# Kernel optimization log

Measured on AMD Instinct MI355X. Metric: run time of the kernel, lower is better.

## Reference

```python
import jax, jax.numpy as jnp
import numpy as np

VOCAB = 128000
D = 256
N_BUBBLES = 256
N_EQ_STEPS = 5
SEQ_LEN = 512
ETA = 0.1      # relaxation rate toward input
KAPPA = 0.05   # mean-field coupling between bubbles


def setup_inputs() -> dict:
    key = jax.random.key(0)
    k1, k2, k3 = jax.random.split(key, 3)
    embed = jax.random.normal(k1, (VOCAB, D), dtype=jnp.float32)
    bubbles = jax.random.normal(k2, (N_BUBBLES, D), dtype=jnp.float32)
    memory_decay_base = jnp.asarray(0.8, dtype=jnp.float32)
    novelty_sensitivity = jnp.asarray(1.0, dtype=jnp.float32)
    tokens = jax.random.randint(k3, (SEQ_LEN,), 0, VOCAB, dtype=jnp.int64)
    return {"embed": embed, "bubbles": bubbles,
            "memory_decay_base": memory_decay_base,
            "novelty_sensitivity": novelty_sensitivity,
            "tokens": tokens}


def _foam_forward(x, bubbles):
    """x: [d]. Equilibrate bubble states, build density matrix, eigen-spectrum."""
    s = bubbles  # [n_bubbles, d]
    for _ in range(N_EQ_STEPS):  # fixed small hyperparam loop
        s = s + ETA * (x[None, :] - s) + KAPPA * (s.mean(axis=0, keepdims=True) - s)
        s = s / (jnp.linalg.norm(s, axis=-1, keepdims=True) + 1e-10)
    rho = (s.T @ s) / s.shape[0]  # [d, d] PSD, trace ~ 1
    w = jnp.linalg.eigvalsh(rho)  # ascending eigenvalues [d]
    w = jnp.clip(w, 0.0)
    output_dist = w / (w.sum() + 1e-10)
    return s, output_dist


def reference(embed, bubbles, memory_decay_base, novelty_sensitivity, tokens):
    sens = jnp.abs(novelty_sensitivity)

    def step(memory, tok):
        x = embed[tok]                      # [d]
        mem_mean = memory.mean(axis=0)      # [d]
        mem_norm = jnp.linalg.norm(mem_mean) + 1e-10
        x_norm = jnp.linalg.norm(x) + 1e-10
        novelty = jnp.where(mem_norm > 1e-8,
                            1.0 - jnp.dot(x, mem_mean) / (x_norm * mem_norm),
                            1.0)
        decay = jax.nn.sigmoid(memory_decay_base - sens * novelty)
        x_with_memory = x + decay * mem_mean
        eq, output_dist = _foam_forward(x_with_memory, bubbles)
        memory = decay * memory + (1.0 - decay) * eq
        return memory, output_dist

    memory0 = jnp.zeros_like(bubbles)  # [n_bubbles, d]
    _, dists = jax.lax.scan(step, memory0, tokens)
    return dists  # [seq_len, d] per-step eigenvalue distributions of rho
```

## Files before the change

kernel.cpp:

```cpp
#include <hip/hip_runtime.h>
#include <hip/hip_fp16.h>
#include <math.h>

#define SEQ 512
#define ETA 0.1f
#define KAPPA 0.05f
#define AA 0.85f

typedef _Float16 f16x8 __attribute__((ext_vector_type(8)));
typedef float f32x4 __attribute__((ext_vector_type(4)));

#define WS_G    ((size_t)0)
#define WS_GD   ((size_t)65536)
#define WS_M0   ((size_t)65792)
#define WS_BX   ((size_t)66048)
#define WS_X2   ((size_t)197120)
#define WS_ZS   ((size_t)197632)
#define WS_YS   ((size_t)328704)
#define WS_GS   ((size_t)459776)
#define WS_HS   ((size_t)984064)
#define WS_ALS  ((size_t)986112)
#define WS_BETS ((size_t)1117184)
#define WS_CT   ((size_t)1772544)

__device__ __forceinline__ float wred_sum(float v) {
#pragma unroll
  for (int m = 1; m < 64; m <<= 1) v += __shfl_xor(v, m, 64);
  return v;
}
__device__ __forceinline__ float wred_min(float v) {
#pragma unroll
  for (int m = 1; m < 64; m <<= 1) v = fminf(v, __shfl_xor(v, m, 64));
  return v;
}
__device__ __forceinline__ float wred_max(float v) {
#pragma unroll
  for (int m = 1; m < 64; m <<= 1) v = fmaxf(v, __shfl_xor(v, m, 64));
  return v;
}
__device__ __forceinline__ float psum32(float v) {
  v += __shfl_xor(v, 2, 64);
  v += __shfl_xor(v, 4, 64);
  v += __shfl_xor(v, 8, 64);
  v += __shfl_xor(v, 16, 64);
  v += __shfl_xor(v, 32, 64);
  return v;
}
__device__ __forceinline__ float rfl(float x) {
  return __builtin_bit_cast(float, __builtin_amdgcn_readfirstlane(__builtin_bit_cast(int, x)));
}

#define G_LIST(X) X(0) X(1) X(2) X(3) X(4) X(5) X(6) X(7) \
                  X(8) X(9) X(10) X(11) X(12) X(13) X(14) X(15) \
                  X(16) X(17) X(18) X(19) X(20) X(21) X(22) X(23) \
                  X(24) X(25) X(26) X(27) X(28) X(29) X(30) X(31)

__global__ void k0_gram(const float* __restrict__ B, float* __restrict__ ws) {
  float* G = ws + WS_G;
  float* Gd = ws + WS_GD;
  __shared__ float bi[256];
  const int i = blockIdx.x, j = threadIdx.x;
  bi[j] = B[(size_t)i * 256 + j];
  __syncthreads();
  float a0 = 0.f, a1 = 0.f, a2 = 0.f, a3 = 0.f;
#pragma unroll
  for (int c = 0; c < 256; c += 4) {
    float4 b4 = *(const float4*)&B[(size_t)j * 256 + c];
    a0 = fmaf(bi[c + 0], b4.x, a0);
    a1 = fmaf(bi[c + 1], b4.y, a1);
    a2 = fmaf(bi[c + 2], b4.z, a2);
    a3 = fmaf(bi[c + 3], b4.w, a3);
  }
  float acc = (a0 + a1) + (a2 + a3);
  G[(size_t)i * 256 + j] = acc;
  if (i == j) Gd[i] = acc;
}

__global__ void k0_m0(const float* __restrict__ B, float* __restrict__ ws) {
  float* M0 = ws + WS_M0;
  const int d = threadIdx.x;
  float acc = 0.f;
  for (int i = 0; i < 256; ++i) acc += B[(size_t)i * 256 + d];
  M0[d] = acc * (1.0f / 256.0f);
}

__global__ void k0_bx(const float* __restrict__ B, const float* __restrict__ embed,
                      const int* __restrict__ toks, float* __restrict__ ws) {
  float* BX = ws + WS_BX;
  float* X2 = ws + WS_X2;
  __shared__ float xs[256];
  __shared__ float red[4];
  const int t = blockIdx.x, i = threadIdx.x;
  const int lane = i & 63, wid = i >> 6;
  const int tok = toks[t];
  float xv = embed[(size_t)tok * 256 + i];
  xs[i] = xv;
  float p = wred_sum(xv * xv);
  if (lane == 0) red[wid] = p;
  __syncthreads();
  if (i == 0) X2[t] = red[0] + red[1] + red[2] + red[3];
  float a0 = 0.f, a1 = 0.f, a2 = 0.f, a3 = 0.f;
#pragma unroll
  for (int c = 0; c < 256; c += 4) {
    float4 b4 = *(const float4*)&B[(size_t)i * 256 + c];
    a0 = fmaf(xs[c + 0], b4.x, a0);
    a1 = fmaf(xs[c + 1], b4.y, a1);
    a2 = fmaf(xs[c + 2], b4.z, a2);
    a3 = fmaf(xs[c + 3], b4.w, a3);
  }
  BX[(size_t)t * 256 + i] = (a0 + a1) + (a2 + a3);
}

__global__ __launch_bounds__(512)
__attribute__((amdgpu_waves_per_eu(2, 2)))
void k1_seq(
    const float* __restrict__ embed, const int* __restrict__ toks,
    const float* __restrict__ mdbp, const float* __restrict__ sensp,
    float* __restrict__ ws) {
  const int tid = threadIdx.x;
  const int lane = tid & 63;
  const int i = tid >> 1, h = tid & 1;
  const float* G = ws + WS_G;
  const float* Gd = ws + WS_GD;
  const float* BX = ws + WS_BX;
  const float* X2 = ws + WS_X2;
  float* ZS = ws + WS_ZS;
  float* YS = ws + WS_YS;
  float* GS = ws + WS_GS;
  float* HS = ws + WS_HS;
  float* ALS = ws + WS_ALS;
  float* BETS = ws + WS_BETS;

  __shared__ __align__(16) float gcur[256];
  __shared__ float dresb[2][8];
  __shared__ float bbarb[2][8];

  const float4* gp = (const float4*)(G + (size_t)i * 256 + (size_t)h * 128);
#define DECLG(J) float4 Gr##J = gp[J];
  G_LIST(DECLG)
#undef DECLG
  const float Gdi = Gd[i];
  const float mdb = rfl(mdbp[0]);
  const float sens = fabsf(rfl(sensp[0]));

  float q0i;
  {
    float s = 0.f;
#define SUMG(J) s += (Gr##J.x + Gr##J.y) + (Gr##J.z + Gr##J.w);
    G_LIST(SUMG)
#undef SUMG
    s += __shfl_xor(s, 1, 64);
    q0i = s * (1.0f / 256.0f);
  }

  float x_c = embed[(size_t)toks[0] * 256 + i];
  float bx_c = BX[i];
  float x2_c = rfl(X2[0]);

  if (tid < 16) dresb[tid >> 3][tid & 7] = 0.f;
  else if (tid < 32) bbarb[(tid - 16) >> 3][tid & 7] = 0.f;
  __syncthreads();
  {
    float v = h ? (bx_c * (1.0f / 256.0f)) : (q0i * (1.0f / 256.0f));
    v = psum32(v);
    if (lane == h) atomicAdd(&dresb[0][h], v);
  }
  __syncthreads();
  const float c00 = rfl(dresb[0][0]);
  float mbx = rfl(dresb[0][1]);

  float Zi = 0.f, yi = 0.f, wi = 0.f;
  float mm2 = 0.f, mw = 0.f, dotxm = 0.f;

  float dec = 1.0f / (1.0f + expf(-(mdb - sens)));
  float od = 1.0f - dec;
  float ri = bx_c;
  float XM2 = x2_c;
  float mean_r = mbx;
  if (h == 0) ZS[i] = 0.f;
  else YS[i] = x_c;

  float gh[6], Ggh[6], hhv[6], bmat[5], xmm[5], alpha;
  gh[0] = 1.0f / 256.0f; Ggh[0] = q0i; hhv[0] = 0.f;
  {
    const float xmm0 = mean_r;
    const float tki = ETA * ri + KAPPA * q0i;
    const float CC00 = (ETA * ETA) * XM2 + 2.f * (ETA * KAPPA) * xmm0 +
                       (KAPPA * KAPPA) * c00;
    const float n2 = fmaxf(AA * AA * Gdi + 2.f * AA * tki + CC00, 0.f);
    const float inv = 1.0f / (sqrtf(n2) + 1e-10f);
    bmat[0] = inv; alpha = AA * inv; xmm[0] = xmm0;
  }
  if (h == 0) gcur[i] = alpha;
  {
    float bv = h ? 0.f : bmat[0];
    bv = psum32(bv);
    if (lane == 0) atomicAdd(&bbarb[1][0], bv);
  }
  __syncthreads();
  int pq = 1;

#pragma unroll 1
  for (int t = 0; t < SEQ; ++t) {
    const int tn = (t + 1 < SEQ) ? (t + 1) : t;
    const int tokn = toks[tn];
    const float x_n = embed[(size_t)tokn * 256 + i];
    const float bx_n = BX[(size_t)tn * 256 + i];
    const float x2_n = rfl(X2[tn]);
    float q5sav = 0.f;

#pragma unroll
    for (int k = 1; k <= 5; ++k) {
      if (tid < 8) dresb[1 - pq][tid] = 0.f;
      else if (tid < 16) bbarb[1 - pq][tid - 8] = 0.f;
      float4 av = {0.f, 0.f, 0.f, 0.f};
      const float4* gc4 = (const float4*)&gcur[h * 128];
#define MVG(J) { const float4 g4 = gc4[J]; \
      av.x = fmaf(Gr##J.x, g4.x, av.x); av.y = fmaf(Gr##J.y, g4.y, av.y); \
      av.z = fmaf(Gr##J.z, g4.z, av.z); av.w = fmaf(Gr##J.w, g4.w, av.w); }
      G_LIST(MVG)
#undef MVG
      float M = (av.x + av.y) + (av.z + av.w);
      M += __shfl_xor(M, 1, 64);
      float hk = 0.f, gk = alpha * (1.0f / 256.0f), Ggk = M * (1.0f / 256.0f);
#pragma unroll
      for (int l = 0; l < 5; ++l)
        if (l < k) {
          const float bb = rfl(bbarb[pq][l]) * (1.0f / 256.0f);
          hk += bb * (ETA + KAPPA * hhv[l]);
          gk = fmaf(KAPPA * bb, gh[l], gk);
          Ggk = fmaf(KAPPA * bb, Ggh[l], Ggk);
        }
      const float qk = Ggk + hk * ri;
      gh[k] = gk; Ggh[k] = Ggk; hhv[k] = hk;
      if (k <= 4) {
        if (h == 1) GS[(size_t)(k - 1) * (SEQ * 256) + (size_t)t * 256 + i] = gk;
        if (tid == 0) HS[(size_t)(k - 1) * SEQ + t] = hk;
      }
      float vv[8];
      if (k < 5) {
#pragma unroll
        for (int l = 0; l < 8; ++l) {
          if (l <= k) vv[l] = gk * (Ggh[l] + hhv[l] * ri);
          else if (l == k + 1) vv[l] = ri * gk;
          else vv[l] = 0.f;
        }
      } else {
        q5sav = qk;
        vv[0] = gk * qk;
        vv[1] = ri * gk;
        vv[2] = wi * gk;
        vv[3] = qk * (1.0f / 256.0f);
        vv[4] = bx_n * Zi + x_n * yi;
        vv[5] = bx_n * gk;
        vv[6] = x_n * x_c;
        vv[7] = bx_n * (1.0f / 256.0f);
      }
      const int nv = (k < 5) ? (k + 2) : 8;
      const int ulim = (k < 5) ? (k + 2) : 4;
      float red4[4] = {0.f, 0.f, 0.f, 0.f};
#pragma unroll
      for (int u = 0; u < 4; ++u)
        if (u < ulim) red4[u] = psum32(h ? vv[4 + u] : vv[u]);
      if (lane == h) {
#pragma unroll
        for (int u = 0; u < 4; ++u) {
          const int sl = h * 4 + u;
          if (sl < nv) atomicAdd(&dresb[pq][sl], red4[u]);
        }
      }
      __syncthreads();

      if (k < 5) {
        float dres[7];
#pragma unroll
        for (int l = 0; l < 7; ++l)
          if (l <= k + 1) dres[l] = rfl(dresb[pq][l]);
        const float xmmk = dres[k + 1] + hk * XM2;
        const float tki = ETA * ri + KAPPA * qk;
        float sc = alpha * tki;
#pragma unroll
        for (int jj = 0; jj < 4; ++jj)
          if (jj < k) {
            const float MMjk = dres[jj] + hk * xmm[jj];
            const float CCjk = (ETA * ETA) * XM2 + (ETA * KAPPA) * (xmm[jj] + xmmk) +
                               (KAPPA * KAPPA) * MMjk;
            sc = fmaf(bmat[jj], CCjk, sc);
          }
        const float MMkk = dres[k] + hk * xmmk;
        const float CCkk = (ETA * ETA) * XM2 + 2.f * (ETA * KAPPA) * xmmk +
                           (KAPPA * KAPPA) * MMkk;
        const float n2 = fmaxf(AA * AA + 2.f * AA * sc + CCkk, 0.f);
        const float inv = 1.0f / (sqrtf(n2) + 1e-10f);
#pragma unroll
        for (int jj = 0; jj < 4; ++jj)
          if (jj < k) bmat[jj] *= AA * inv;
        bmat[k] = inv;
        alpha *= AA * inv;
        xmm[k] = xmmk;
        if (k == 4) {
          if (h == 1) {
            ALS[(size_t)t * 256 + i] = alpha;
            BETS[(size_t)1 * (SEQ * 256) + (size_t)t * 256 + i] = bmat[1];
            BETS[(size_t)3 * (SEQ * 256) + (size_t)t * 256 + i] = bmat[3];
          } else {
            BETS[(size_t)0 * (SEQ * 256) + (size_t)t * 256 + i] = bmat[0];
            BETS[(size_t)2 * (SEQ * 256) + (size_t)t * 256 + i] = bmat[2];
            BETS[(size_t)4 * (SEQ * 256) + (size_t)t * 256 + i] = bmat[4];
          }
        }
        if (h == 0) gcur[i] = alpha;
        float rb0 = h ? bmat[1] : bmat[0];
        float rb1 = h ? ((k >= 3) ? bmat[3] : 0.f) : ((k >= 2) ? bmat[2] : 0.f);
        float rb2 = h ? 0.f : ((k >= 4) ? bmat[4] : 0.f);
        rb0 = psum32(rb0);
        if (k >= 2) rb1 = psum32(rb1);
        if (k >= 4) rb2 = psum32(rb2);
        if (lane == h) {
          atomicAdd(&bbarb[1 - pq][h], rb0);
          if (2 + h <= k) atomicAdd(&bbarb[1 - pq][2 + h], rb1);
          if (4 + h <= k) atomicAdd(&bbarb[1 - pq][4 + h], rb2);
        }
        __syncthreads();
        pq ^= 1;
      } else {
        float dr[8];
#pragma unroll
        for (int l = 0; l < 8; ++l) dr[l] = rfl(dresb[pq][l]);
        const float h5 = hhv[5];
        const float g5 = gh[5];
        const float q5 = q5sav;
        const float xmm5 = dr[1] + h5 * XM2;
        const float m52 = dr[0] + h5 * xmm5;
        const float cmm5 = dr[2] + h5 * (dotxm + dec * mm2);
        const float lamc = dec * (1.0f + od * h5);
        Zi = lamc * Zi + od * g5;
        yi = lamc * yi + od * h5 * x_c;
        wi = dec * wi + od * q5;
        mm2 = fmaxf(dec * dec * mm2 + 2.f * dec * od * cmm5 + od * od * m52, 0.f);
        mw = dec * mw + od * dr[3];
        dotxm = lamc * dr[4] + od * (dr[5] + h5 * dr[6]);
        mbx = dr[7];
        x_c = x_n; bx_c = bx_n; x2_c = x2_n;
        const float memnorm = sqrtf(mm2) + 1e-10f;
        const float xnorm = sqrtf(x2_c) + 1e-10f;
        const float nov = (memnorm > 1e-8f) ? (1.0f - dotxm / (xnorm * memnorm)) : 1.0f;
        dec = 1.0f / (1.0f + expf(-(mdb - sens * nov)));
        od = 1.0f - dec;
        ri = bx_c + dec * wi;
        XM2 = x2_c + 2.f * dec * dotxm + dec * dec * mm2;
        mean_r = mbx + dec * mw;
        if (t + 1 < SEQ) {
          if (h == 0) ZS[(size_t)(t + 1) * 256 + i] = dec * Zi;
          else YS[(size_t)(t + 1) * 256 + i] = x_c + dec * yi;
        }
        const float xmm0 = mean_r;
        const float tki = ETA * ri + KAPPA * q0i;
        const float CC00 = (ETA * ETA) * XM2 + 2.f * (ETA * KAPPA) * xmm0 +
                           (KAPPA * KAPPA) * c00;
        const float n2 = fmaxf(AA * AA * Gdi + 2.f * AA * tki + CC00, 0.f);
        const float inv = 1.0f / (sqrtf(n2) + 1e-10f);
        bmat[0] = inv; alpha = AA * inv; xmm[0] = xmm0;
        if (h == 0) gcur[i] = alpha;
        float bv = h ? 0.f : bmat[0];
        bv = psum32(bv);
        if (lane == 0) atomicAdd(&bbarb[1 - pq][0], bv);
        __syncthreads();
        pq ^= 1;
      }
    }
  }
}

__global__ void k15_cvec(const float* __restrict__ B, float* __restrict__ ws) {
  const float* ZS = ws + WS_ZS;
  const float* YS = ws + WS_YS;
  const float* GS = ws + WS_GS;
  const float* HS = ws + WS_HS;
  const float* M0 = ws + WS_M0;
  float* CT = ws + WS_CT;
  const int t = blockIdx.x, d = threadIdx.x;
  __shared__ float zs[256], g1[256], g2[256], g3[256], g4[256];
  zs[d] = ZS[(size_t)t * 256 + d];
  g1[d] = GS[0 * (SEQ * 256) + (size_t)t * 256 + d];
  g2[d] = GS[1 * (SEQ * 256) + (size_t)t * 256 + d];
  g3[d] = GS[2 * (SEQ * 256) + (size_t)t * 256 + d];
  g4[d] = GS[3 * (SEQ * 256) + (size_t)t * 256 + d];
  __syncthreads();
  float xa = 0.f, b1 = 0.f, b2 = 0.f, b3 = 0.f, b4 = 0.f;
  for (int ii = 0; ii < 256; ++ii) {
    const float Bv = B[(size_t)ii * 256 + d];
    xa = fmaf(zs[ii], Bv, xa);
    b1 = fmaf(g1[ii], Bv, b1);
    b2 = fmaf(g2[ii], Bv, b2);
    b3 = fmaf(g3[ii], Bv, b3);
    b4 = fmaf(g4[ii], Bv, b4);
  }
  const float xm = YS[(size_t)t * 256 + d] + xa;
  float* ctt = CT + (size_t)t * 1280;
  ctt[0 * 256 + d] = ETA * xm + KAPPA * M0[d];
  const float h1 = HS[0 * SEQ + t], h2 = HS[1 * SEQ + t];
  const float h3 = HS[2 * SEQ + t], h4 = HS[3 * SEQ + t];
  ctt[1 * 256 + d] = (ETA + KAPPA * h1) * xm + KAPPA * b1;
  ctt[2 * 256 + d] = (ETA + KAPPA * h2) * xm + KAPPA * b2;
  ctt[3 * 256 + d] = (ETA + KAPPA * h3) * xm + KAPPA * b3;
  ctt[4 * 256 + d] = (ETA + KAPPA * h4) * xm + KAPPA * b4;
}

__global__ __launch_bounds__(1024, 4) void k2_eig(
    const float* __restrict__ B, const float* __restrict__ ws,
    float* __restrict__ out) {
  const int t = blockIdx.x;
  const int tid = threadIdx.x;
  const int lane = tid & 63, wid = tid >> 6;
  const float* CT = ws + WS_CT + (size_t)t * 1280;
  const float* ALS = ws + WS_ALS + (size_t)t * 256;
  const float* BETS = ws + WS_BETS;

  __shared__ __align__(16) unsigned char bigbuf[135168];
  _Float16* sT = (_Float16*)bigbuf;
  float* pk = (float*)bigbuf;
  __shared__ __align__(16) float ct[1280];
  __shared__ float vx[256], pv[256], qv[256];
  __shared__ float dd[256], ee[256], e2[256], lamv[256];
  __shared__ float red[16];

  for (int idx = tid; idx < 1280; idx += 1024) ct[idx] = CT[idx];
  __syncthreads();

  {
    const int r = tid >> 2, q = tid & 3;
    const float al = ALS[r];
    const float be0 = BETS[(size_t)0 * (SEQ * 256) + (size_t)t * 256 + r];
    const float be1 = BETS[(size_t)1 * (SEQ * 256) + (size_t)t * 256 + r];
    const float be2 = BETS[(size_t)2 * (SEQ * 256) + (size_t)t * 256 + r];
    const float be3 = BETS[(size_t)3 * (SEQ * 256) + (size_t)t * 256 + r];
    const float be4 = BETS[(size_t)4 * (SEQ * 256) + (size_t)t * 256 + r];
#pragma unroll
    for (int j4 = 0; j4 < 16; ++j4) {
      const int d0 = q * 64 + j4 * 4;
      const float4 Bv = *(const float4*)&B[(size_t)r * 256 + d0];
      const float4 c0 = *(const float4*)&ct[0 * 256 + d0];
      const float4 c1 = *(const float4*)&ct[1 * 256 + d0];
      const float4 c2 = *(const float4*)&ct[2 * 256 + d0];
      const float4 c3 = *(const float4*)&ct[3 * 256 + d0];
      const float4 c4 = *(const float4*)&ct[4 * 256 + d0];
      const float s0 = al * Bv.x + be0 * c0.x + be1 * c1.x + be2 * c2.x + be3 * c3.x + be4 * c4.x;
      const float s1 = al * Bv.y + be0 * c0.y + be1 * c1.y + be2 * c2.y + be3 * c3.y + be4 * c4.y;
      const float s2 = al * Bv.z + be0 * c0.z + be1 * c1.z + be2 * c2.z + be3 * c3.z + be4 * c4.z;
      const float s3 = al * Bv.w + be0 * c0.w + be1 * c1.w + be2 * c2.w + be3 * c3.w + be4 * c4.w;
      sT[(size_t)(d0 + 0) * 264 + r] = (_Float16)s0;
      sT[(size_t)(d0 + 1) * 264 + r] = (_Float16)s1;
      sT[(size_t)(d0 + 2) * 264 + r] = (_Float16)s2;
      sT[(size_t)(d0 + 3) * 264 + r] = (_Float16)s3;
    }
  }
  __syncthreads();

  f32x4 acc[4][4];
#pragma unroll
  for (int ti = 0; ti < 4; ++ti)
#pragma unroll
    for (int tj = 0; tj < 4; ++tj) {
      f32x4 z = {0.f, 0.f, 0.f, 0.f};
      acc[ti][tj] = z;
    }
  {
    const int Ib = (wid >> 2) * 4, Jb = (wid & 3) * 4;
    const int mr = lane & 15, kg = lane >> 4;
#pragma unroll 1
    for (int kb = 0; kb < 8; ++kb) {
      const int ko = kb * 32 + kg * 8;
      f16x8 aF[4], bF[4];
#pragma unroll
      for (int ti = 0; ti < 4; ++ti)
        aF[ti] = *(const f16x8*)&sT[(size_t)((Ib + ti) * 16 + mr) * 264 + ko];
#pragma unroll
      for (int tj = 0; tj < 4; ++tj)
        bF[tj] = *(const f16x8*)&sT[(size_t)((Jb + tj) * 16 + mr) * 264 + ko];
#pragma unroll
      for (int ti = 0; ti < 4; ++ti)
#pragma unroll
        for (int tj = 0; tj < 4; ++tj)
          acc[ti][tj] = __builtin_amdgcn_mfma_f32_16x16x32_f16(aF[ti], bF[tj], acc[ti][tj], 0, 0, 0);
    }
  }
  __syncthreads();
  {
    const int Ib = (wid >> 2) * 4, Jb = (wid & 3) * 4;
    const int cn = lane & 15, rg = lane >> 4;
#pragma unroll
    for (int ti = 0; ti < 4; ++ti)
#pragma unroll
      for (int tj = 0; tj < 4; ++tj) {
        const int C = (Jb + tj) * 16 + cn;
        const int Rb = (Ib + ti) * 16 + rg * 4;
#pragma unroll
        for (int rr = 0; rr < 4; ++rr) {
          const int R = Rb + rr;
          if (R >= C) pk[R * (R + 1) / 2 + C] = acc[ti][tj][rr] * (1.0f / 256.0f);
        }
      }
  }
  __syncthreads();

#pragma unroll 1
  for (int j = 0; j < 254; ++j) {
    const int m = 255 - j;
    const float x0 = pk[(j + 1) * (j + 2) / 2 + j];
    float ps = 0.f;
    if (tid < m) {
      const int gr = j + 1 + tid;
      const float xv_ = pk[gr * (gr + 1) / 2 + j];
      vx[tid] = xv_;
      ps = xv_ * xv_;
    }
    ps = wred_sum(ps);
    if (lane == 0) red[wid] = ps;
    __syncthreads();
    float sig2 = 0.f;
#pragma unroll
    for (int w = 0; w < 16; ++w) sig2 += red[w];
    const float sig = sqrtf(sig2);
    const float sg = (x0 >= 0.f) ? 1.f : -1.f;
    const bool live = (sig2 > 1e-26f);
    const float beta = live ? (1.0f / (sig * (sig + fabsf(x0)))) : 0.f;
    const float v0 = live ? (x0 + sg * sig) : 0.f;
    if (tid == 0) {
      dd[j] = pk[j * (j + 1) / 2 + j];
      ee[j] = live ? (-sg * sig) : x0;
      vx[0] = v0;
    }
    __syncthreads();
    {
      const int ri_ = tid >> 2, qd = tid & 3;
      float acc2 = 0.f;
      if (ri_ < m) {
        const int gr = j + 1 + ri_;
        const int c0 = (m * qd) >> 2, c1 = (m * (qd + 1)) >> 2;
        const int rowbase = gr * (gr + 1) / 2 + (j + 1);
        const int clend = min(c1, ri_ + 1);
        for (int c = c0; c < clend; ++c) acc2 = fmaf(pk[rowbase + c], vx[c], acc2);
        const int cu = max(c0, ri_ + 1);
        if (cu < c1) {
          int gc = j + 1 + cu;
          int ub = gc * (gc + 1) / 2 + gr;
          int stp = gc + 1;
          for (int c = cu; c < c1; ++c) { acc2 = fmaf(pk[ub], vx[c], acc2); ub += stp; ++stp; }
        }
      }
      acc2 += __shfl_xor(acc2, 1, 64);
      acc2 += __shfl_xor(acc2, 2, 64);
      float vpp = 0.f;
      if ((tid & 3) == 0 && (tid >> 2) < m) { pv[tid >> 2] = acc2; vpp = acc2 * vx[tid >> 2]; }
      vpp = wred_sum(vpp);
      if (lane == 0) red[wid] = vpp;
    }
    __syncthreads();
    float vtp = 0.f;
#pragma unroll
    for (int w = 0; w < 16; ++w) vtp += red[w];
    const float gamma = 0.5f * beta * beta * vtp;
    if (tid < m) qv[tid] = beta * pv[tid] - gamma * vx[tid];
    __syncthreads();
    {
      const int Q = tid >> 2, qd = tid & 3;
      const int i2 = m - 1 - Q;
      if (Q <= i2 && Q < m) {
        {
          const int gr = j + 1 + Q;
          const int rb = gr * (gr + 1) / 2 + (j + 1);
          const float vi = vx[Q], qi = qv[Q];
          const int cs = (qd * (Q + 1)) >> 2, ce = ((qd + 1) * (Q + 1)) >> 2;
          for (int c = cs; c < ce; ++c) pk[rb + c] -= vi * qv[c] + qi * vx[c];
        }
        if (i2 > Q) {
          const int gr = j + 1 + i2;
          const int rb = gr * (gr + 1) / 2 + (j + 1);
          const float vi = vx[i2], qi = qv[i2];
          const int cs = (qd * (i2 + 1)) >> 2, ce = ((qd + 1) * (i2 + 1)) >> 2;
          for (int c = cs; c < ce; ++c) pk[rb + c] -= vi * qv[c] + qi * vx[c];
        }
      }
    }
    __syncthreads();
  }
  if (tid == 0) {
    dd[254] = pk[254 * 255 / 2 + 254];
    dd[255] = pk[255 * 256 / 2 + 255];
    ee[254] = pk[255 * 256 / 2 + 254];
    ee[255] = 0.f;
  }
  __syncthreads();
  if (tid < 256) e2[tid] = ee[tid] * ee[tid];
  __syncthreads();
  float glo = 1e30f, ghi = -1e30f;
  if (tid < 256) {
    const float rad = fabsf(ee[tid]) + ((tid > 0) ? fabsf(ee[tid - 1]) : 0.f);
    glo = dd[tid] - rad;
    ghi = dd[tid] + rad;
  }
  {
    float v = wred_min(glo);
    if (lane == 0) red[wid] = v;
    __syncthreads();
    float lo0 = 1e30f;
#pragma unroll
    for (int w = 0; w < 16; ++w) lo0 = fminf(lo0, red[w]);
    __syncthreads();
    v = wred_max(ghi);
    if (lane == 0) red[wid] = v;
    __syncthreads();
    float hi0 = -1e30f;
#pragma unroll
    for (int w = 0; w < 16; ++w) hi0 = fmaxf(hi0, red[w]);
    lo0 -= 1e-3f + 1e-3f * fabsf(lo0);
    hi0 += 1e-3f + 1e-3f * fabsf(hi0);
    if (tid < 256) {
      float lo = lo0, hi = hi0;
      for (int it = 0; it < 21; ++it) {
        const float x = 0.5f * (lo + hi);
        int cnt = 0;
        float qq = dd[0] - x;
        cnt += (qq < 0.f);
        for (int ii = 1; ii < 256; ++ii) {
          float dn = qq;
          if (fabsf(dn) < 1e-25f) dn = (dn < 0.f) ? -1e-25f : 1e-25f;
          qq = (dd[ii] - x) - e2[ii - 1] * __builtin_amdgcn_rcpf(dn);
          cnt += (qq < 0.f);
        }
        if (cnt >= tid + 1) hi = x; else lo = x;
      }
      lamv[tid] = fmaxf(0.5f * (lo + hi), 0.f);
    }
  }
  __syncthreads();
  float sv = (tid < 256) ? lamv[tid] : 0.f;
  sv = wred_sum(sv);
  if (lane == 0) red[wid] = sv;
  __syncthreads();
  float S = 0.f;
#pragma unroll
  for (int w = 0; w < 16; ++w) S += red[w];
  if (tid < 256) out[(size_t)t * 256 + tid] = lamv[tid] / (S + 1e-10f);
}

extern "C" void kernel_launch(void* const* d_in, const int* in_sizes, int n_in,
                              void* d_out, int out_size, void* d_ws, size_t ws_size,
                              hipStream_t stream) {
  const float* embed = (const float*)d_in[0];
  const float* B = (const float*)d_in[1];
  const float* mdb = (const float*)d_in[2];
  const float* sens = (const float*)d_in[3];
  const int* toks = (const int*)d_in[4];
  float* out = (float*)d_out;
  float* ws = (float*)d_ws;

  k0_gram<<<dim3(256), dim3(256), 0, stream>>>(B, ws);
  k0_m0<<<dim3(1), dim3(256), 0, stream>>>(B, ws);
  k0_bx<<<dim3(SEQ), dim3(256), 0, stream>>>(B, embed, toks, ws);
  k1_seq<<<dim3(1), dim3(512), 0, stream>>>(embed, toks, mdb, sens, ws);
  k15_cvec<<<dim3(SEQ), dim3(256), 0, stream>>>(B, ws);
  k2_eig<<<dim3(SEQ), dim3(1024), 0, stream>>>(B, ws, out);
}
```

Baseline: 10.63 ms.

## Split sequential kernel's Gram matvec across four thread groups with deferred partial sums

The single-block sequential kernel grows from 512 to 1024 threads, and each row of the register-resident Gram matrix is split into four 64-column chunks instead of two halves. Partial matvec results go to a shared buffer and are combined only after the existing barrier. The per-step reduction algebra is reworked to use these partial sums, so the cross-lane shuffle on the critical path goes away. This halves register pressure per thread and shortens each matvec, but adds more wave reductions and atomics and doubles the waves taking part in every barrier.

```diff
diff --git a/kernel.cpp b/kernel.cpp
--- a/kernel.cpp
+++ b/kernel.cpp
@@ -38,22 +38,12 @@
   for (int m = 1; m < 64; m <<= 1) v = fmaxf(v, __shfl_xor(v, m, 64));
   return v;
 }
-__device__ __forceinline__ float psum32(float v) {
-  v += __shfl_xor(v, 2, 64);
-  v += __shfl_xor(v, 4, 64);
-  v += __shfl_xor(v, 8, 64);
-  v += __shfl_xor(v, 16, 64);
-  v += __shfl_xor(v, 32, 64);
-  return v;
-}
 __device__ __forceinline__ float rfl(float x) {
   return __builtin_bit_cast(float, __builtin_amdgcn_readfirstlane(__builtin_bit_cast(int, x)));
 }
 
 #define G_LIST(X) X(0) X(1) X(2) X(3) X(4) X(5) X(6) X(7) \
-                  X(8) X(9) X(10) X(11) X(12) X(13) X(14) X(15) \
-                  X(16) X(17) X(18) X(19) X(20) X(21) X(22) X(23) \
-                  X(24) X(25) X(26) X(27) X(28) X(29) X(30) X(31)
+                  X(8) X(9) X(10) X(11) X(12) X(13) X(14) X(15)
 
 __global__ void k0_gram(const float* __restrict__ B, float* __restrict__ ws) {
   float* G = ws + WS_G;
@@ -111,15 +101,15 @@
   BX[(size_t)t * 256 + i] = (a0 + a1) + (a2 + a3);
 }
 
-__global__ __launch_bounds__(512)
-__attribute__((amdgpu_waves_per_eu(2, 2)))
+__global__ __launch_bounds__(1024)
+__attribute__((amdgpu_waves_per_eu(4, 4)))
 void k1_seq(
     const float* __restrict__ embed, const int* __restrict__ toks,
     const float* __restrict__ mdbp, const float* __restrict__ sensp,
     float* __restrict__ ws) {
   const int tid = threadIdx.x;
   const int lane = tid & 63;
-  const int i = tid >> 1, h = tid & 1;
+  const int i = tid & 255, c = tid >> 8;
   const float* G = ws + WS_G;
   const float* Gd = ws + WS_GD;
   const float* BX = ws + WS_BX;
@@ -132,10 +122,11 @@
   float* BETS = ws + WS_BETS;
 
   __shared__ __align__(16) float gcur[256];
+  __shared__ float pbuf[4][264];
   __shared__ float dresb[2][8];
   __shared__ float bbarb[2][8];
 
-  const float4* gp = (const float4*)(G + (size_t)i * 256 + (size_t)h * 128);
+  const float4* gp = (const float4*)(G + (size_t)i * 256 + (size_t)c * 64);
 #define DECLG(J) float4 Gr##J = gp[J];
   G_LIST(DECLG)
 #undef DECLG
@@ -143,27 +134,33 @@
   const float mdb = rfl(mdbp[0]);
   const float sens = fabsf(rfl(sensp[0]));
 
-  float q0i;
+  float Gghp0;
   {
     float s = 0.f;
 #define SUMG(J) s += (Gr##J.x + Gr##J.y) + (Gr##J.z + Gr##J.w);
     G_LIST(SUMG)
 #undef SUMG
-    s += __shfl_xor(s, 1, 64);
-    q0i = s * (1.0f / 256.0f);
-  }
+    Gghp0 = s * (1.0f / 256.0f);
+  }
+  if (tid < 8) dresb[0][tid] = 0.f;
+  else if (tid < 16) dresb[1][tid - 8] = 0.f;
+  else if (tid < 24) bbarb[0][tid - 16] = 0.f;
+  else if (tid < 32) bbarb[1][tid - 24] = 0.f;
+  pbuf[c][i] = Gghp0;
+  __syncthreads();
+  const float q0i = pbuf[0][i] + pbuf[1][i] + pbuf[2][i] + pbuf[3][i];
 
   float x_c = embed[(size_t)toks[0] * 256 + i];
   float bx_c = BX[i];
   float x2_c = rfl(X2[0]);
 
-  if (tid < 16) dresb[tid >> 3][tid & 7] = 0.f;
-  else if (tid < 32) bbarb[(tid - 16) >> 3][tid & 7] = 0.f;
-  __syncthreads();
-  {
-    float v = h ? (bx_c * (1.0f / 256.0f)) : (q0i * (1.0f / 256.0f));
-    v = psum32(v);
-    if (lane == h) atomicAdd(&dresb[0][h], v);
+  if (c == 0) {
+    float v0 = wred_sum(q0i * (1.0f / 256.0f));
+    float v1 = wred_sum(bx_c * (1.0f / 256.0f));
+    if (lane == 0) {
+      atomicAdd(&dresb[0][0], v0);
+      atomicAdd(&dresb[0][1], v1);
+    }
   }
   __syncthreads();
   const float c00 = rfl(dresb[0][0]);
@@ -177,11 +174,11 @@
   float ri = bx_c;
   float XM2 = x2_c;
   float mean_r = mbx;
-  if (h == 0) ZS[i] = 0.f;
-  else YS[i] = x_c;
-
-  float gh[6], Ggh[6], hhv[6], bmat[5], xmm[5], alpha;
-  gh[0] = 1.0f / 256.0f; Ggh[0] = q0i; hhv[0] = 0.f;
+  if (c == 0) ZS[i] = 0.f;
+  else if (c == 1) YS[i] = x_c;
+
+  float gh[6], Gghp[6], hhv[6], bmat[5], xmm[5], alpha;
+  gh[0] = 1.0f / 256.0f; Gghp[0] = Gghp0; hhv[0] = 0.f;
   {
     const float xmm0 = mean_r;
     const float tki = ETA * ri + KAPPA * q0i;
@@ -191,11 +188,10 @@
     const float inv = 1.0f / (sqrtf(n2) + 1e-10f);
     bmat[0] = inv; alpha = AA * inv; xmm[0] = xmm0;
   }
-  if (h == 0) gcur[i] = alpha;
-  {
-    float bv = h ? 0.f : bmat[0];
-    bv = psum32(bv);
-    if (lane == 0) atomicAdd(&bbarb[1][0], bv);
+  if (c == 0) {
+    gcur[i] = alpha;
+    float bv = wred_sum(bmat[0]);
+    if (lane == 0) atomicAdd(&bbarb[1][0], bv * (1.0f / 256.0f));
   }
   __syncthreads();
   int pq = 1;
@@ -214,80 +210,87 @@
       if (tid < 8) dresb[1 - pq][tid] = 0.f;
       else if (tid < 16) bbarb[1 - pq][tid - 8] = 0.f;
       float4 av = {0.f, 0.f, 0.f, 0.f};
-      const float4* gc4 = (const float4*)&gcur[h * 128];
+      const float4* gc4 = (const float4*)&gcur[c * 64];
 #define MVG(J) { const float4 g4 = gc4[J]; \
       av.x = fmaf(Gr##J.x, g4.x, av.x); av.y = fmaf(Gr##J.y, g4.y, av.y); \
       av.z = fmaf(Gr##J.z, g4.z, av.z); av.w = fmaf(Gr##J.w, g4.w, av.w); }
       G_LIST(MVG)
 #undef MVG
-      float M = (av.x + av.y) + (av.z + av.w);
-      M += __shfl_xor(M, 1, 64);
-      float hk = 0.f, gk = alpha * (1.0f / 256.0f), Ggk = M * (1.0f / 256.0f);
+      const float M = (av.x + av.y) + (av.z + av.w);
+      float hk = 0.f, gk = alpha * (1.0f / 256.0f), Ggp = M * (1.0f / 256.0f);
 #pragma unroll
       for (int l = 0; l < 5; ++l)
         if (l < k) {
-          const float bb = rfl(bbarb[pq][l]) * (1.0f / 256.0f);
+          const float bb = rfl(bbarb[pq][l]);
           hk += bb * (ETA + KAPPA * hhv[l]);
           gk = fmaf(KAPPA * bb, gh[l], gk);
-          Ggk = fmaf(KAPPA * bb, Ggh[l], Ggk);
-        }
-      const float qk = Ggk + hk * ri;
-      gh[k] = gk; Ggh[k] = Ggk; hhv[k] = hk;
+          Ggp = fmaf(KAPPA * bb, Gghp[l], Ggp);
+        }
+      gh[k] = gk; Gghp[k] = Ggp; hhv[k] = hk;
       if (k <= 4) {
-        if (h == 1) GS[(size_t)(k - 1) * (SEQ * 256) + (size_t)t * 256 + i] = gk;
+        if (c == 1) GS[(size_t)(k - 1) * (SEQ * 256) + (size_t)t * 256 + i] = gk;
         if (tid == 0) HS[(size_t)(k - 1) * SEQ + t] = hk;
       }
-      float vv[8];
+      pbuf[c][i] = Ggp;
       if (k < 5) {
 #pragma unroll
-        for (int l = 0; l < 8; ++l) {
-          if (l <= k) vv[l] = gk * (Ggh[l] + hhv[l] * ri);
-          else if (l == k + 1) vv[l] = ri * gk;
-          else vv[l] = 0.f;
+        for (int l = 0; l < 5; ++l)
+          if (l <= k) {
+            const float s = wred_sum(gk * Gghp[l]);
+            if (lane == 0) atomicAdd(&dresb[pq][l], s);
+          }
+        if (c == 0) {
+          const float s = wred_sum(ri * gk);
+          if (lane == 0) atomicAdd(&dresb[pq][k + 1], s);
         }
       } else {
-        q5sav = qk;
-        vv[0] = gk * qk;
-        vv[1] = ri * gk;
-        vv[2] = wi * gk;
-        vv[3] = qk * (1.0f / 256.0f);
-        vv[4] = bx_n * Zi + x_n * yi;
-        vv[5] = bx_n * gk;
-        vv[6] = x_n * x_c;
-        vv[7] = bx_n * (1.0f / 256.0f);
-      }
-      const int nv = (k < 5) ? (k + 2) : 8;
-      const int ulim = (k < 5) ? (k + 2) : 4;
-      float red4[4] = {0.f, 0.f, 0.f, 0.f};
-#pragma unroll
-      for (int u = 0; u < 4; ++u)
-        if (u < ulim) red4[u] = psum32(h ? vv[4 + u] : vv[u]);
-      if (lane == h) {
-#pragma unroll
-        for (int u = 0; u < 4; ++u) {
-          const int sl = h * 4 + u;
-          if (sl < nv) atomicAdd(&dresb[pq][sl], red4[u]);
+        q5sav = gk;
+        const float s0 = wred_sum(gk * Ggp);
+        const float s3 = wred_sum(Ggp * (1.0f / 256.0f));
+        if (lane == 0) {
+          atomicAdd(&dresb[pq][0], s0);
+          atomicAdd(&dresb[pq][3], s3);
+        }
+        if (c == 0) {
+          const float s1 = wred_sum(ri * gk);
+          const float s2 = wred_sum(wi * gk);
+          const float s4 = wred_sum(bx_n * Zi + x_n * yi);
+          const float s5 = wred_sum(bx_n * gk);
+          const float s6 = wred_sum(x_n * x_c);
+          const float s7 = wred_sum(bx_n * (1.0f / 256.0f));
+          if (lane == 0) {
+            atomicAdd(&dresb[pq][1], s1);
+            atomicAdd(&dresb[pq][2], s2);
+            atomicAdd(&dresb[pq][4], s4);
+            atomicAdd(&dresb[pq][5], s5);
+            atomicAdd(&dresb[pq][6], s6);
+            atomicAdd(&dresb[pq][7], s7);
+          }
         }
       }
       __syncthreads();
 
+      const float hk_ = hhv[k];
+      const float qfull = pbuf[0][i] + pbuf[1][i] + pbuf[2][i] + pbuf[3][i] +
+                          hk_ * ri;
       if (k < 5) {
         float dres[7];
 #pragma unroll
         for (int l = 0; l < 7; ++l)
           if (l <= k + 1) dres[l] = rfl(dresb[pq][l]);
-        const float xmmk = dres[k + 1] + hk * XM2;
-        const float tki = ETA * ri + KAPPA * qk;
+        const float Rk = dres[k + 1];
+        const float xmmk = Rk + hk_ * XM2;
+        const float tki = ETA * ri + KAPPA * qfull;
         float sc = alpha * tki;
 #pragma unroll
         for (int jj = 0; jj < 4; ++jj)
           if (jj < k) {
-            const float MMjk = dres[jj] + hk * xmm[jj];
+            const float MMjk = dres[jj] + hhv[jj] * Rk + hk_ * xmm[jj];
             const float CCjk = (ETA * ETA) * XM2 + (ETA * KAPPA) * (xmm[jj] + xmmk) +
                                (KAPPA * KAPPA) * MMjk;
             sc = fmaf(bmat[jj], CCjk, sc);
           }
-        const float MMkk = dres[k] + hk * xmmk;
+        const float MMkk = dres[k] + hk_ * Rk + hk_ * xmmk;
         const float CCkk = (ETA * ETA) * XM2 + 2.f * (ETA * KAPPA) * xmmk +
                            (KAPPA * KAPPA) * MMkk;
         const float n2 = fmaxf(AA * AA + 2.f * AA * sc + CCkk, 0.f);
@@ -299,46 +302,48 @@
         alpha *= AA * inv;
         xmm[k] = xmmk;
         if (k == 4) {
-          if (h == 1) {
+          if (c == 1) {
+            BETS[(size_t)0 * (SEQ * 256) + (size_t)t * 256 + i] = bmat[0];
+            BETS[(size_t)1 * (SEQ * 256) + (size_t)t * 256 + i] = bmat[1];
+          } else if (c == 2) {
+            BETS[(size_t)2 * (SEQ * 256) + (size_t)t * 256 + i] = bmat[2];
+            BETS[(size_t)3 * (SEQ * 256) + (size_t)t * 256 + i] = bmat[3];
+          } else if (c == 3) {
+            BETS[(size_t)4 * (SEQ * 256) + (size_t)t * 256 + i] = bmat[4];
             ALS[(size_t)t * 256 + i] = alpha;
-            BETS[(size_t)1 * (SEQ * 256) + (size_t)t * 256 + i] = bmat[1];
-            BETS[(size_t)3 * (SEQ * 256) + (size_t)t * 256 + i] = bmat[3];
-          } else {
-            BETS[(size_t)0 * (SEQ * 256) + (size_t)t * 256 + i] = bmat[0];
-            BETS[(size_t)2 * (SEQ * 256) + (size_t)t * 256 + i] = bmat[2];
-            BETS[(size_t)4 * (SEQ * 256) + (size_t)t * 256 + i] = bmat[4];
           }
         }
-        if (h == 0) gcur[i] = alpha;
-        float rb0 = h ? bmat[1] : bmat[0];
-        float rb1 = h ? ((k >= 3) ? bmat[3] : 0.f) : ((k >= 2) ? bmat[2] : 0.f);
-        float rb2 = h ? 0.f : ((k >= 4) ? bmat[4] : 0.f);
-        rb0 = psum32(rb0);
-        if (k >= 2) rb1 = psum32(rb1);
-        if (k >= 4) rb2 = psum32(rb2);
-        if (lane == h) {
-          atomicAdd(&bbarb[1 - pq][h], rb0);
-          if (2 + h <= k) atomicAdd(&bbarb[1 - pq][2 + h], rb1);
-          if (4 + h <= k) atomicAdd(&bbarb[1 - pq][4 + h], rb2);
+        if (c == 0) {
+          gcur[i] = alpha;
+#pragma unroll
+          for (int l = 0; l < 5; ++l)
+            if (l <= k) {
+              const float bv = wred_sum(bmat[l]);
+              if (lane == 0) atomicAdd(&bbarb[1 - pq][l], bv * (1.0f / 256.0f));
+            }
         }
         __syncthreads();
         pq ^= 1;
       } else {
+        const float q5 = qfull;
         float dr[8];
 #pragma unroll
         for (int l = 0; l < 8; ++l) dr[l] = rfl(dresb[pq][l]);
         const float h5 = hhv[5];
         const float g5 = gh[5];
-        const float q5 = q5sav;
-        const float xmm5 = dr[1] + h5 * XM2;
-        const float m52 = dr[0] + h5 * xmm5;
-        const float cmm5 = dr[2] + h5 * (dotxm + dec * mm2);
+        const float B5 = dr[1];
+        const float A5 = dr[0] + h5 * B5;
+        const float C5 = dr[2];
+        const float mq5 = dr[3] + h5 * mean_r;
+        const float xmm5 = B5 + h5 * XM2;
+        const float m52 = A5 + h5 * xmm5;
+        const float cmm5 = C5 + h5 * (dotxm + dec * mm2);
         const float lamc = dec * (1.0f + od * h5);
         Zi = lamc * Zi + od * g5;
         yi = lamc * yi + od * h5 * x_c;
         wi = dec * wi + od * q5;
         mm2 = fmaxf(dec * dec * mm2 + 2.f * dec * od * cmm5 + od * od * m52, 0.f);
-        mw = dec * mw + od * dr[3];
+        mw = dec * mw + od * mq5;
         dotxm = lamc * dr[4] + od * (dr[5] + h5 * dr[6]);
         mbx = dr[7];
         x_c = x_n; bx_c = bx_n; x2_c = x2_n;
@@ -351,8 +356,8 @@
         XM2 = x2_c + 2.f * dec * dotxm + dec * dec * mm2;
         mean_r = mbx + dec * mw;
         if (t + 1 < SEQ) {
-          if (h == 0) ZS[(size_t)(t + 1) * 256 + i] = dec * Zi;
-          else YS[(size_t)(t + 1) * 256 + i] = x_c + dec * yi;
+          if (c == 0) ZS[(size_t)(t + 1) * 256 + i] = dec * Zi;
+          else if (c == 1) YS[(size_t)(t + 1) * 256 + i] = x_c + dec * yi;
         }
         const float xmm0 = mean_r;
         const float tki = ETA * ri + KAPPA * q0i;
@@ -361,10 +366,11 @@
         const float n2 = fmaxf(AA * AA * Gdi + 2.f * AA * tki + CC00, 0.f);
         const float inv = 1.0f / (sqrtf(n2) + 1e-10f);
         bmat[0] = inv; alpha = AA * inv; xmm[0] = xmm0;
-        if (h == 0) gcur[i] = alpha;
-        float bv = h ? 0.f : bmat[0];
-        bv = psum32(bv);
-        if (lane == 0) atomicAdd(&bbarb[1 - pq][0], bv);
+        if (c == 0) {
+          gcur[i] = alpha;
+          const float bv = wred_sum(bmat[0]);
+          if (lane == 0) atomicAdd(&bbarb[1 - pq][0], bv * (1.0f / 256.0f));
+        }
         __syncthreads();
         pq ^= 1;
       }
@@ -659,7 +665,7 @@
   k0_gram<<<dim3(256), dim3(256), 0, stream>>>(B, ws);
   k0_m0<<<dim3(1), dim3(256), 0, stream>>>(B, ws);
   k0_bx<<<dim3(SEQ), dim3(256), 0, stream>>>(B, embed, toks, ws);
-  k1_seq<<<dim3(1), dim3(512), 0, stream>>>(embed, toks, mdb, sens, ws);
+  k1_seq<<<dim3(1), dim3(1024), 0, stream>>>(embed, toks, mdb, sens, ws);
   k15_cvec<<<dim3(SEQ), dim3(256), 0, stream>>>(B, ws);
   k2_eig<<<dim3(SEQ), dim3(1024), 0, stream>>>(B, ws, out);
 }
```

Measured after the change: 36.13 ms. +240.0%, slower.
